# Performance work log

Hardware: AMD Instinct MI355X
Metric: run time of the kernel (lower is better)

Reference implementation:

```python
import jax, jax.numpy as jnp
import numpy as np


def _pairwise_dist(x):
    # x: [B, N, D] -> [B, N, N] Euclidean distances (torch.cdist, p=2)
    sq = jnp.sum(x * x, axis=-1)  # [B, N]
    sq_d = sq[:, :, None] + sq[:, None, :] - 2.0 * jnp.einsum('bnd,bmd->bnm', x, x)
    sq_d = jnp.maximum(sq_d, 0.0)
    # safe sqrt (zero diagonal): avoid NaN by masking
    return jnp.where(sq_d > 0.0, jnp.sqrt(jnp.where(sq_d > 0.0, sq_d, 1.0)), 0.0)


def setup_inputs() -> dict:
    key = jax.random.key(0)
    k1, k2, k3 = jax.random.split(key, 3)
    B, N, D = 8, 2048, 3
    preds = jax.random.normal(k1, (B, N, D), dtype=jnp.float32)
    targets = jax.random.normal(k2, (B, N, D), dtype=jnp.float32)
    adj_matrix = jax.random.randint(k3, (B, N, N), 0, 2).astype(jnp.float32)
    return {"preds": preds, "targets": targets, "adj_matrix": adj_matrix}


def reference(preds, targets, adj_matrix):
    dist_preds = _pairwise_dist(preds)      # [B, N, N]
    dist_targets = _pairwise_dist(targets)  # [B, N, N]
    dist = (dist_preds - dist_targets) * adj_matrix
    return jnp.sum(dist * dist) / jnp.sum(adj_matrix)
```

## Files before the change

kernel.cpp:

```cpp
#include <hip/hip_runtime.h>

#define BQ 8
#define NQ 2048
#define ROWS 8
#define TPB 256
#define NBLK (BQ * (NQ / ROWS))

__global__ __launch_bounds__(TPB) void idla_main(
        const float* __restrict__ preds,
        const float* __restrict__ targets,
        const float* __restrict__ adj,
        float2* __restrict__ partials) {
    __shared__ __attribute__((aligned(16))) float px[NQ], py[NQ], pz[NQ];
    __shared__ __attribute__((aligned(16))) float tx[NQ], ty[NQ], tz[NQ];
    __shared__ float red_sq[TPB / 64], red_ad[TPB / 64];

    const int nb_per_batch = NQ / ROWS;
    const int b  = blockIdx.x / nb_per_batch;
    const int i0 = (blockIdx.x % nb_per_batch) * ROWS;
    const int tid = threadIdx.x;

    const float* pb = preds   + (size_t)b * NQ * 3;
    const float* tb = targets + (size_t)b * NQ * 3;
    for (int e = tid; e < NQ * 3; e += TPB) {
        int j = e / 3;
        int c = e - 3 * j;
        float v = pb[e];
        float w = tb[e];
        if (c == 0)      { px[j] = v; tx[j] = w; }
        else if (c == 1) { py[j] = v; ty[j] = w; }
        else             { pz[j] = v; tz[j] = w; }
    }
    __syncthreads();

    float acc_sq = 0.0f;
    float acc_ad = 0.0f;
    const float* adjb = adj + (size_t)b * NQ * NQ;

    #pragma unroll
    for (int ig = 0; ig < ROWS; ig += 4) {
        float pix[4], piy[4], piz[4], tix[4], tiy[4], tiz[4];
        #pragma unroll
        for (int ii = 0; ii < 4; ii++) {
            int i = i0 + ig + ii;
            pix[ii] = px[i]; piy[ii] = py[i]; piz[ii] = pz[i];
            tix[ii] = tx[i]; tiy[ii] = ty[i]; tiz[ii] = tz[i];
        }
        for (int j0 = tid * 4; j0 < NQ; j0 += TPB * 4) {
            float4 vx = *(const float4*)&px[j0];
            float4 vy = *(const float4*)&py[j0];
            float4 vz = *(const float4*)&pz[j0];
            float4 wx = *(const float4*)&tx[j0];
            float4 wy = *(const float4*)&ty[j0];
            float4 wz = *(const float4*)&tz[j0];
            float jx[4] = {vx.x, vx.y, vx.z, vx.w};
            float jy[4] = {vy.x, vy.y, vy.z, vy.w};
            float jz[4] = {vz.x, vz.y, vz.z, vz.w};
            float ux[4] = {wx.x, wx.y, wx.z, wx.w};
            float uy[4] = {wy.x, wy.y, wy.z, wy.w};
            float uz[4] = {wz.x, wz.y, wz.z, wz.w};

            #pragma unroll
            for (int ii = 0; ii < 4; ii++) {
                int i = i0 + ig + ii;
                float4 a4 = *(const float4*)&adjb[(size_t)i * NQ + j0];
                float av[4] = {a4.x, a4.y, a4.z, a4.w};
                #pragma unroll
                for (int jj = 0; jj < 4; jj++) {
                    float dx = pix[ii] - jx[jj];
                    float dy = piy[ii] - jy[jj];
                    float dz = piz[ii] - jz[jj];
                    float sp = fmaf(dx, dx, fmaf(dy, dy, dz * dz));
                    float ex = tix[ii] - ux[jj];
                    float ey = tiy[ii] - uy[jj];
                    float ez = tiz[ii] - uz[jj];
                    float st = fmaf(ex, ex, fmaf(ey, ey, ez * ez));
                    float r  = __builtin_amdgcn_sqrtf(sp * st);
                    float t  = fmaf(-2.0f, r, sp + st);
                    float aa = av[jj] * av[jj];
                    acc_sq = fmaf(t, aa, acc_sq);
                    acc_ad += av[jj];
                }
            }
        }
    }

    #pragma unroll
    for (int off = 32; off > 0; off >>= 1) {
        acc_sq += __shfl_down(acc_sq, off, 64);
        acc_ad += __shfl_down(acc_ad, off, 64);
    }
    const int wave = tid >> 6;
    if ((tid & 63) == 0) { red_sq[wave] = acc_sq; red_ad[wave] = acc_ad; }
    __syncthreads();
    if (tid == 0) {
        float s_sq = 0.0f, s_ad = 0.0f;
        #pragma unroll
        for (int w = 0; w < TPB / 64; w++) { s_sq += red_sq[w]; s_ad += red_ad[w]; }
        partials[blockIdx.x] = make_float2(s_sq, s_ad);
    }
}

__global__ __launch_bounds__(256) void idla_reduce(
        const float2* __restrict__ partials, float* __restrict__ out) {
    double s = 0.0, a = 0.0;
    for (int i = threadIdx.x; i < NBLK; i += 256) {
        float2 p = partials[i];
        s += (double)p.x;
        a += (double)p.y;
    }
    #pragma unroll
    for (int off = 32; off > 0; off >>= 1) {
        s += __shfl_down(s, off, 64);
        a += __shfl_down(a, off, 64);
    }
    __shared__ double rs[4], ra[4];
    const int wave = threadIdx.x >> 6;
    if ((threadIdx.x & 63) == 0) { rs[wave] = s; ra[wave] = a; }
    __syncthreads();
    if (threadIdx.x == 0) {
        double ts = rs[0] + rs[1] + rs[2] + rs[3];
        double ta = ra[0] + ra[1] + ra[2] + ra[3];
        out[0] = (float)(ts / ta);
    }
}

extern "C" void kernel_launch(void* const* d_in, const int* in_sizes, int n_in,
                              void* d_out, int out_size, void* d_ws, size_t ws_size,
                              hipStream_t stream) {
    const float* preds   = (const float*)d_in[0];
    const float* targets = (const float*)d_in[1];
    const float* adj     = (const float*)d_in[2];
    float2* partials = (float2*)d_ws;
    float*  out      = (float*)d_out;

    hipLaunchKernelGGL(idla_main, dim3(NBLK), dim3(TPB), 0, stream,
                       preds, targets, adj, partials);
    hipLaunchKernelGGL(idla_reduce, dim3(1), dim3(256), 0, stream, partials, out);
}
```

Measured before the change: 210.2 us.

## Drop shared-memory staging; read point coords directly from global per tile

Removes the per-block staging of all 2048 preds/targets points into LDS, which was repeated by all 2048 blocks along with a barrier. Each thread now loads its 4 j-points straight from global memory as three float4s and deinterleaves them in registers. The loop order is swapped so that all 8 adjacency rows per j-tile are loaded up front, giving more memory-level parallelism. Launch bounds now request 4 blocks per CU; the cost is repeated global or L2 reads of the coordinates and higher register pressure.

```diff
diff --git a/kernel.cpp b/kernel.cpp
--- a/kernel.cpp
+++ b/kernel.cpp
@@ -5,14 +5,14 @@
 #define ROWS 8
 #define TPB 256
 #define NBLK (BQ * (NQ / ROWS))
+#define JTILE (TPB * 4)
+#define NJT (NQ / JTILE)
 
-__global__ __launch_bounds__(TPB) void idla_main(
+__global__ __launch_bounds__(TPB, 4) void idla_main(
         const float* __restrict__ preds,
         const float* __restrict__ targets,
         const float* __restrict__ adj,
         float2* __restrict__ partials) {
-    __shared__ __attribute__((aligned(16))) float px[NQ], py[NQ], pz[NQ];
-    __shared__ __attribute__((aligned(16))) float tx[NQ], ty[NQ], tz[NQ];
     __shared__ float red_sq[TPB / 64], red_ad[TPB / 64];
 
     const int nb_per_batch = NQ / ROWS;
@@ -20,67 +20,53 @@
     const int i0 = (blockIdx.x % nb_per_batch) * ROWS;
     const int tid = threadIdx.x;
 
-    const float* pb = preds   + (size_t)b * NQ * 3;
-    const float* tb = targets + (size_t)b * NQ * 3;
-    for (int e = tid; e < NQ * 3; e += TPB) {
-        int j = e / 3;
-        int c = e - 3 * j;
-        float v = pb[e];
-        float w = tb[e];
-        if (c == 0)      { px[j] = v; tx[j] = w; }
-        else if (c == 1) { py[j] = v; ty[j] = w; }
-        else             { pz[j] = v; tz[j] = w; }
-    }
-    __syncthreads();
+    const float* pb   = preds   + (size_t)b * NQ * 3;
+    const float* tb   = targets + (size_t)b * NQ * 3;
+    const float* adjb = adj     + (size_t)b * NQ * NQ;
 
     float acc_sq = 0.0f;
     float acc_ad = 0.0f;
-    const float* adjb = adj + (size_t)b * NQ * NQ;
 
     #pragma unroll
-    for (int ig = 0; ig < ROWS; ig += 4) {
-        float pix[4], piy[4], piz[4], tix[4], tiy[4], tiz[4];
+    for (int jt = 0; jt < NJT; ++jt) {
+        const int j0 = jt * JTILE + tid * 4;
+        const float4* pj = (const float4*)(pb + 3 * j0);
+        const float4* tj = (const float4*)(tb + 3 * j0);
+        float4 f0 = pj[0], f1 = pj[1], f2 = pj[2];
+        float4 g0 = tj[0], g1 = tj[1], g2 = tj[2];
+        float jx[4] = {f0.x, f0.w, f1.z, f2.y};
+        float jy[4] = {f0.y, f1.x, f1.w, f2.z};
+        float jz[4] = {f0.z, f1.y, f2.x, f2.w};
+        float ux[4] = {g0.x, g0.w, g1.z, g2.y};
+        float uy[4] = {g0.y, g1.x, g1.w, g2.z};
+        float uz[4] = {g0.z, g1.y, g2.x, g2.w};
+
+        float4 a4[ROWS];
         #pragma unroll
-        for (int ii = 0; ii < 4; ii++) {
-            int i = i0 + ig + ii;
-            pix[ii] = px[i]; piy[ii] = py[i]; piz[ii] = pz[i];
-            tix[ii] = tx[i]; tiy[ii] = ty[i]; tiz[ii] = tz[i];
-        }
-        for (int j0 = tid * 4; j0 < NQ; j0 += TPB * 4) {
-            float4 vx = *(const float4*)&px[j0];
-            float4 vy = *(const float4*)&py[j0];
-            float4 vz = *(const float4*)&pz[j0];
-            float4 wx = *(const float4*)&tx[j0];
-            float4 wy = *(const float4*)&ty[j0];
-            float4 wz = *(const float4*)&tz[j0];
-            float jx[4] = {vx.x, vx.y, vx.z, vx.w};
-            float jy[4] = {vy.x, vy.y, vy.z, vy.w};
-            float jz[4] = {vz.x, vz.y, vz.z, vz.w};
-            float ux[4] = {wx.x, wx.y, wx.z, wx.w};
-            float uy[4] = {wy.x, wy.y, wy.z, wy.w};
-            float uz[4] = {wz.x, wz.y, wz.z, wz.w};
+        for (int r = 0; r < ROWS; ++r)
+            a4[r] = *(const float4*)&adjb[(size_t)(i0 + r) * NQ + j0];
 
+        #pragma unroll
+        for (int r = 0; r < ROWS; ++r) {
+            const int i = i0 + r;
+            const float pix = pb[3*i], piy = pb[3*i+1], piz = pb[3*i+2];
+            const float tix = tb[3*i], tiy = tb[3*i+1], tiz = tb[3*i+2];
+            float av[4] = {a4[r].x, a4[r].y, a4[r].z, a4[r].w};
             #pragma unroll
-            for (int ii = 0; ii < 4; ii++) {
-                int i = i0 + ig + ii;
-                float4 a4 = *(const float4*)&adjb[(size_t)i * NQ + j0];
-                float av[4] = {a4.x, a4.y, a4.z, a4.w};
-                #pragma unroll
-                for (int jj = 0; jj < 4; jj++) {
-                    float dx = pix[ii] - jx[jj];
-                    float dy = piy[ii] - jy[jj];
-                    float dz = piz[ii] - jz[jj];
-                    float sp = fmaf(dx, dx, fmaf(dy, dy, dz * dz));
-                    float ex = tix[ii] - ux[jj];
-                    float ey = tiy[ii] - uy[jj];
-                    float ez = tiz[ii] - uz[jj];
-                    float st = fmaf(ex, ex, fmaf(ey, ey, ez * ez));
-                    float r  = __builtin_amdgcn_sqrtf(sp * st);
-                    float t  = fmaf(-2.0f, r, sp + st);
-                    float aa = av[jj] * av[jj];
-                    acc_sq = fmaf(t, aa, acc_sq);
-                    acc_ad += av[jj];
-                }
+            for (int jj = 0; jj < 4; ++jj) {
+                float dx = pix - jx[jj];
+                float dy = piy - jy[jj];
+                float dz = piz - jz[jj];
+                float sp = fmaf(dx, dx, fmaf(dy, dy, dz * dz));
+                float ex = tix - ux[jj];
+                float ey = tiy - uy[jj];
+                float ez = tiz - uz[jj];
+                float st = fmaf(ex, ex, fmaf(ey, ey, ez * ez));
+                float rt = __builtin_amdgcn_sqrtf(sp * st);
+                float t  = fmaf(-2.0f, rt, sp + st);
+                float aa = av[jj] * av[jj];
+                acc_sq = fmaf(t, aa, acc_sq);
+                acc_ad += av[jj];
             }
         }
     }
```

Result: faster. 194.2 us (-7.6%).
